# Optimization experiments

Measured on AMD Instinct MI355X. Metric: run time of the kernel, lower is better.

Reference implementation:

```python
import jax, jax.numpy as jnp
import numpy as np

B, N = 16, 4096
NUM_POINTS = (1024, 256)
NUM_SAMPLE = (32, 64)
CH = ((3, 64, 64, 128), (128, 128, 128, 256))


def setup_inputs() -> dict:
    key = jax.random.key(0)
    ks = iter(jax.random.split(key, 64))
    inp = {"points": jax.random.normal(next(ks), (B, 3, N), jnp.float32)}
    for li, ch in enumerate(CH, 1):
        cin = ch[0] + 3  # xyz-offset concat adds 3 channels at layer input
        for ci in range(len(ch) - 1):
            cout = ch[ci + 1]
            inp[f"w{li}{ci}"] = jax.random.normal(next(ks), (cout, cin), jnp.float32) * (1.0 / np.sqrt(cin))
            inp[f"g{li}{ci}"] = 1.0 + 0.1 * jax.random.normal(next(ks), (cout,), jnp.float32)
            inp[f"b{li}{ci}"] = 0.1 * jax.random.normal(next(ks), (cout,), jnp.float32)
            cin = cout
    return inp


def _fps(points_b3n, npoint):
    # furthest point sampling, seeded at index 0 (matches CUDA furthest_point_sample)
    pts = points_b3n.transpose(0, 2, 1)  # [B, N, 3]
    Bc, Nc, _ = pts.shape
    idx0 = jnp.zeros((Bc,), jnp.int32)
    d0 = jnp.full((Bc, Nc), jnp.inf, pts.dtype)

    def step(carry, _):
        dist, last = carry
        lp = jnp.take_along_axis(pts, jnp.broadcast_to(last[:, None, None], (Bc, 1, 3)), axis=1)  # [B,1,3]
        dist = jnp.minimum(dist, jnp.sum((pts - lp) ** 2, -1))
        nxt = jnp.argmax(dist, -1).astype(jnp.int32)
        return (dist, nxt), nxt

    _, rest = jax.lax.scan(step, (d0, idx0), None, length=npoint - 1)
    return jnp.concatenate([idx0[None], rest], 0).T  # [B, npoint]


def _knn(k, points_b3n, query_b3m):
    p = points_b3n.transpose(0, 2, 1)  # [B, N, 3]
    q = query_b3m.transpose(0, 2, 1)   # [B, M, 3]
    d = (jnp.sum(q * q, -1)[:, :, None]
         - 2.0 * jnp.einsum('bmc,bnc->bmn', q, p)
         + jnp.sum(p * p, -1)[:, None, :])  # [B, M, N]
    _, idx = jax.lax.top_k(-d, k)
    return idx  # [B, M, k]


def _group(x_bcn, idx_bmk):
    # gather neighbors: [B, C, N], [B, M, K] -> [B, C, M, K]
    return jax.vmap(lambda x, i: x[:, i])(x_bcn, idx_bmk)


def _forward(points, params):
    feats = points  # feats=None branch
    outs = []
    for npoint, nsample, layer_params in zip(NUM_POINTS, NUM_SAMPLE, params):
        Bc = points.shape[0]
        fps_idx = _fps(points, npoint)  # [B, npoint]
        prop = jnp.take_along_axis(points, jnp.broadcast_to(fps_idx[:, None, :], (Bc, 3, npoint)), axis=2)
        gidx = _knn(nsample, points, prop)  # [B, npoint, nsample]
        gp = _group(points, gidx)           # [B, 3, M, K]
        gpn = gp - prop[..., None]
        gf = _group(feats, gidx)            # [B, C, M, K]
        x = jnp.concatenate([gpn, gf], axis=1)
        for (W, g, b) in layer_params:      # 1x1 Conv2d + folded BN(eval) + ReLU
            x = jnp.einsum('bcmk,oc->bomk', x, W)
            x = jax.nn.relu(x * g[None, :, None, None] + b[None, :, None, None])
        feats = jnp.max(x, axis=-1)  # max-pool over nsample
        points = prop
        outs += [prop, feats]
    return tuple(outs)  # (points1, feats1, points2, feats2)


def reference(points, w10, g10, b10, w11, g11, b11, w12, g12, b12,
              w20, g20, b20, w21, g21, b21, w22, g22, b22):
    params = [[(w10, g10, b10), (w11, g11, b11), (w12, g12, b12)],
              [(w20, g20, b20), (w21, g21, b21), (w22, g22, b22)]]
    return _forward(points, params)
```

## Files before the change

kernel.cpp:

```cpp
#include <hip/hip_runtime.h>
#include <math.h>

#define NB   16

#define O_P1 0
#define O_F1 (16*3*1024)
#define O_P2 (O_F1 + 16*128*1024)
#define O_F2 (O_P2 + 16*3*256)

#define WS_GIDX1 0
#define WS_GIDX2 (WS_GIDX1 + 16*1024*32*4)
#define WS_W1T   (WS_GIDX2 + 16*256*64*4)
#define WS_W2T   (WS_W1T  + 6*64*4)
#define WS_W3T   (WS_W2T  + 64*64*4)
#define WS_W1H   (WS_W3T  + 64*128*4)
#define WS_W2H   (WS_W1H  + 128*160*2)
#define WS_W3H   (WS_W2H  + 128*128*2)
#define WS_PTS4  (WS_W3H  + 256*128*2)
#define WS_P14   (WS_PTS4 + 16*4096*16)

#define DEVINL __device__ __forceinline__
typedef unsigned long long u64;
typedef _Float16 f16x8 __attribute__((ext_vector_type(8)));
typedef float f32x4 __attribute__((ext_vector_type(4)));

DEVINL float4 f4fma(float w, float4 v, float4 a) {
    a.x = fmaf(w, v.x, a.x); a.y = fmaf(w, v.y, a.y);
    a.z = fmaf(w, v.z, a.z); a.w = fmaf(w, v.w, a.w);
    return a;
}
DEVINL float4 f4relub(float4 a, float b) {
    float4 r;
    r.x = fmaxf(a.x + b, 0.f); r.y = fmaxf(a.y + b, 0.f);
    r.z = fmaxf(a.z + b, 0.f); r.w = fmaxf(a.w + b, 0.f);
    return r;
}
DEVINL float f4max(float4 a) { return fmaxf(fmaxf(a.x, a.y), fmaxf(a.z, a.w)); }

DEVINL unsigned fkey(float f) {
    unsigned u = __float_as_uint(f);
    return (u & 0x80000000u) ? ~u : (u | 0x80000000u);
}

DEVINL u64 shflx64(u64 v, int m) {
    unsigned lo = __shfl_xor((unsigned)v, m);
    unsigned hi = __shfl_xor((unsigned)(v >> 32), m);
    return ((u64)hi << 32) | lo;
}

template<int CTRL, int RMASK>
DEVINL unsigned dpp_addstep(unsigned v) {
    unsigned t = (unsigned)__builtin_amdgcn_update_dpp(0, (int)v, CTRL, RMASK, 0xF, true);
    return v + t;
}
DEVINL unsigned wave_scan_add(unsigned v) {
    v = dpp_addstep<0x111, 0xF>(v);
    v = dpp_addstep<0x112, 0xF>(v);
    v = dpp_addstep<0x114, 0xF>(v);
    v = dpp_addstep<0x118, 0xF>(v);
    v = dpp_addstep<0x142, 0xA>(v);
    v = dpp_addstep<0x143, 0xC>(v);
    return v;
}

template<int N, int NP> struct __align__(16) FpsS {
    float4 spts[N];
    int sel[NP];
    u64 rbuf[2][4];
};
struct __align__(16) KnnS {
    unsigned hist[2048];
    unsigned ckey[1024];
    int      cidx[1024];
    unsigned wpart[4];
    unsigned sbin, sKb, scnt, cntL;
};
struct __align__(16) Mlp1S {
    float sw1[6*64], sw2[64*64];
    float sb1[64], sb2[64], sb3[128];
    float sx[6*32], sh1[64*36], sh2[64*36];
    float spm[128*4], sout[128*8];
    int   sgi[32];
    float sq[3];
};

DEVINL void prep_impl(int e0,
    const float* __restrict__ w10, const float* __restrict__ g10,
    const float* __restrict__ w11, const float* __restrict__ g11,
    const float* __restrict__ w12, const float* __restrict__ g12,
    const float* __restrict__ w20, const float* __restrict__ g20,
    const float* __restrict__ w21, const float* __restrict__ g21,
    const float* __restrict__ w22, const float* __restrict__ g22,
    float* __restrict__ w1t, float* __restrict__ w2t, float* __restrict__ w3t,
    _Float16* __restrict__ W1h, _Float16* __restrict__ W2h, _Float16* __restrict__ W3h)
{
    if (e0 < 384)  { int o = e0/6,   i = e0%6;   w1t [i*64  + o] = w10[e0]*g10[o]; return; }
    e0 -= 384;
    if (e0 < 4096) { int o = e0/64,  i = e0%64;  w2t [i*64  + o] = w11[e0]*g11[o]; return; }
    e0 -= 4096;
    if (e0 < 8192) { int o = e0/64,  i = e0%64;  w3t [i*128 + o] = w12[e0]*g12[o]; return; }
    e0 -= 8192;
    if (e0 < 20480){ int o = e0/160, i = e0%160;
                     float v = (i < 131) ? w20[o*131 + i]*g20[o] : 0.f;
                     W1h[e0] = (_Float16)v; return; }
    e0 -= 20480;
    if (e0 < 16384){ W2h[e0] = (_Float16)(w21[e0]*g21[e0/128]); return; }
    e0 -= 16384;
    if (e0 < 32768){ W3h[e0] = (_Float16)(w22[e0]*g22[e0/128]); return; }
}

template<int N, int NP>
DEVINL void fps_impl(FpsS<N, NP>& sm, const float* __restrict__ pts,
                     float* __restrict__ prop, int b, float4* pack_out)
{
    constexpr int NT = 256;
    constexpr int PT = N / NT;
    int tid = threadIdx.x;
    const float* p = pts + (size_t)b * 3 * N;
    for (int n = tid; n < N; n += NT) {
        float x = p[n], y = p[N+n], z = p[2*N+n];
        sm.spts[n] = make_float4(x, y, z, 0.f);
        if (pack_out) {
            float s = __fadd_rn(__fadd_rn(__fmul_rn(x,x), __fmul_rn(y,y)), __fmul_rn(z,z));
            pack_out[(size_t)b*N + n] = make_float4(x, y, z, s);
        }
    }
    __syncthreads();

    float lx[PT], ly[PT], lz[PT], ld[PT];
    int base = tid * PT;
#pragma unroll
    for (int j = 0; j < PT; ++j) {
        float4 q = sm.spts[base+j];
        lx[j] = q.x; ly[j] = q.y; lz[j] = q.z;
        ld[j] = __builtin_inff();
    }
    if (tid == 0) sm.sel[0] = 0;
    float4 qp = sm.spts[0];
    for (int s = 1; s < NP; ++s) {
        float qx = qp.x, qy = qp.y, qz = qp.z;
        float bd = -1.0f; int bi = 0x7FFFFFFF;
#pragma unroll
        for (int j = 0; j < PT; ++j) {
            float dx = __fsub_rn(lx[j], qx);
            float dy = __fsub_rn(ly[j], qy);
            float dz = __fsub_rn(lz[j], qz);
            float dd = __fadd_rn(__fadd_rn(__fmul_rn(dx,dx), __fmul_rn(dy,dy)), __fmul_rn(dz,dz));
            float v = fminf(ld[j], dd);
            ld[j] = v;
            if (v > bd) { bd = v; bi = base + j; }
        }
        u64 pk = ((u64)__float_as_uint(bd) << 32) | (unsigned)(~bi);
#pragma unroll
        for (int mk = 1; mk < 64; mk <<= 1) {
            u64 o = shflx64(pk, mk);
            if (o > pk) pk = o;
        }
        if ((tid & 63) == 0) sm.rbuf[s & 1][tid >> 6] = pk;
        __syncthreads();
        u64 g = sm.rbuf[s & 1][0];
#pragma unroll
        for (int w = 1; w < 4; ++w) { u64 o = sm.rbuf[s & 1][w]; if (o > g) g = o; }
        int last = (int)(~(unsigned)g);
        qp = sm.spts[last];
        if (tid == 0) sm.sel[s] = last;
    }
    __syncthreads();
    for (int m = tid; m < NP; m += NT) {
        float4 q = sm.spts[sm.sel[m]];
        prop[(size_t)b*3*NP + m]        = q.x;
        prop[(size_t)b*3*NP + NP + m]   = q.y;
        prop[(size_t)b*3*NP + 2*NP + m] = q.z;
    }
}

template<int N, int K, int M>
DEVINL void knn_impl(KnnS& sm, const float4* __restrict__ pts4,
                     const float* __restrict__ qry, int* __restrict__ gidx, int bm)
{
    int tid = threadIdx.x, lane = tid & 63, wid = tid >> 6;
    int b = bm / M, m = bm % M;
    const float4* p4 = pts4 + (size_t)b * N;
    float qx = qry[(size_t)b*3*M + m];
    float qy = qry[(size_t)b*3*M + M + m];
    float qz = qry[(size_t)b*3*M + 2*M + m];
    float sqq = __fadd_rn(__fadd_rn(__fmul_rn(qx,qx), __fmul_rn(qy,qy)), __fmul_rn(qz,qz));

    for (int e = tid; e < 2048; e += 256) sm.hist[e] = 0;
    if (tid == 0) { sm.scnt = 0; sm.cntL = 0; sm.sbin = 2047u; sm.sKb = 0; }
    __syncthreads();
    for (int n = tid; n < N; n += 256) {
        float4 pp = p4[n];
        float dot = __fadd_rn(__fadd_rn(__fmul_rn(qx,pp.x), __fmul_rn(qy,pp.y)), __fmul_rn(qz,pp.z));
        float d = __fadd_rn(__fsub_rn(sqq, __fmul_rn(2.0f, dot)), pp.w);
        atomicAdd(&sm.hist[fkey(d) >> 21], 1u);
    }
    __syncthreads();
    unsigned hloc[8], s8 = 0;
#pragma unroll
    for (int j = 0; j < 8; ++j) { hloc[j] = sm.hist[tid*8 + j]; s8 += hloc[j]; }
    unsigned sc = wave_scan_add(s8);
    if (lane == 63) sm.wpart[wid] = sc;
    __syncthreads();
    unsigned woff = 0;
    for (int w = 0; w < wid; ++w) woff += sm.wpart[w];
    unsigned cumEnd = sc + woff;
    unsigned cbase = cumEnd - s8;
    if ((unsigned)K > cbase && (unsigned)K <= cumEnd) {
        unsigned run = cbase;
#pragma unroll
        for (int j = 0; j < 8; ++j) {
            if ((unsigned)K > run && (unsigned)K <= run + hloc[j]) { sm.sbin = (unsigned)(tid*8 + j); sm.sKb = run; }
            run += hloc[j];
        }
    }
    __syncthreads();
    unsigned bin1 = sm.sbin;
    unsigned Kb   = sm.sKb;
    int* gout = gidx + ((size_t)b * M + m) * K;
    for (int n = tid; n < N; n += 256) {
        float4 pp = p4[n];
        float dot = __fadd_rn(__fadd_rn(__fmul_rn(qx,pp.x), __fmul_rn(qy,pp.y)), __fmul_rn(qz,pp.z));
        float d = __fadd_rn(__fsub_rn(sqq, __fmul_rn(2.0f, dot)), pp.w);
        unsigned k = fkey(d), pfx = k >> 21;
        if (pfx < bin1) {
            unsigned pos = atomicAdd(&sm.cntL, 1u);
            if (pos < (unsigned)K) gout[pos] = n;
        } else if (pfx == bin1) {
            unsigned pos = atomicAdd(&sm.scnt, 1u);
            if (pos < 1024u) { sm.ckey[pos] = k; sm.cidx[pos] = n; }
        }
    }
    __syncthreads();
    int cnt = (int)sm.scnt; if (cnt > 1024) cnt = 1024;
    int need = K - (int)Kb;
    if (tid < 64) {
        for (int c = lane; c < cnt; c += 64) {
            unsigned mk = sm.ckey[c]; int mi = sm.cidx[c];
            int rank = 0;
            for (int l = 0; l < cnt; ++l) {
                unsigned ok = sm.ckey[l];
                rank += (ok < mk || (ok == mk && sm.cidx[l] < mi)) ? 1 : 0;
            }
            if (rank < need && (int)Kb + rank < K) gout[Kb + rank] = mi;
        }
    }
}

DEVINL void mlp1_impl(Mlp1S& sm,
    const float* __restrict__ pts,
    const float* __restrict__ q,
    const int*   __restrict__ gidx,
    const float* __restrict__ w1t, const float* __restrict__ w2t, const float* __restrict__ w3t,
    const float* __restrict__ b1, const float* __restrict__ b2, const float* __restrict__ b3,
    float* __restrict__ out, int blk)
{
    int tid = threadIdx.x;
    for (int e = tid; e < 6*64;   e += 256) sm.sw1[e] = w1t[e];
    for (int e = tid; e < 64*64;  e += 256) sm.sw2[e] = w2t[e];
    if (tid < 64) { sm.sb1[tid] = b1[tid]; sm.sb2[tid] = b2[tid]; }
    else if (tid < 192) sm.sb3[tid-64] = b3[tid-64];

    int pid0 = blk * 8;
    int b = pid0 >> 10, m0 = pid0 & 1023;
    int c = tid & 63, kq = tid >> 6, kb = kq * 8;
    __syncthreads();

    for (int it = 0; it < 8; ++it) {
        int m = m0 + it;
        if (tid < 32) sm.sgi[tid] = gidx[((size_t)b*1024 + m)*32 + tid];
        else if (tid < 35) sm.sq[tid-32] = q[((size_t)b*3 + (tid-32))*1024 + m];
        __syncthreads();
        if (tid < 192) {
            int cc = tid >> 5, k = tid & 31;
            int gi = sm.sgi[k];
            const float* pb = pts + (size_t)b*3*4096;
            float v = (cc < 3) ? (pb[cc*4096 + gi] - sm.sq[cc]) : pb[(cc-3)*4096 + gi];
            sm.sx[cc*32 + k] = v;
        }
        __syncthreads();
        float4 a0 = make_float4(0,0,0,0), a1 = make_float4(0,0,0,0);
#pragma unroll
        for (int i = 0; i < 6; ++i) {
            float w = sm.sw1[i*64 + c];
            a0 = f4fma(w, *(const float4*)&sm.sx[i*32 + kb],     a0);
            a1 = f4fma(w, *(const float4*)&sm.sx[i*32 + kb + 4], a1);
        }
        {
            float bias = sm.sb1[c];
            *(float4*)&sm.sh1[c*36 + kb]     = f4relub(a0, bias);
            *(float4*)&sm.sh1[c*36 + kb + 4] = f4relub(a1, bias);
        }
        __syncthreads();
        a0 = make_float4(0,0,0,0); a1 = make_float4(0,0,0,0);
#pragma unroll 4
        for (int i = 0; i < 64; ++i) {
            float w = sm.sw2[i*64 + c];
            a0 = f4fma(w, *(const float4*)&sm.sh1[i*36 + kb],     a0);
            a1 = f4fma(w, *(const float4*)&sm.sh1[i*36 + kb + 4], a1);
        }
        {
            float bias = sm.sb2[c];
            *(float4*)&sm.sh2[c*36 + kb]     = f4relub(a0, bias);
            *(float4*)&sm.sh2[c*36 + kb + 4] = f4relub(a1, bias);
        }
        __syncthreads();
        float4 aA0 = make_float4(0,0,0,0), aA1 = make_float4(0,0,0,0);
        float4 aB0 = make_float4(0,0,0,0), aB1 = make_float4(0,0,0,0);
#pragma unroll 4
        for (int i = 0; i < 64; ++i) {
            float wA = w3t[i*128 + c], wB = w3t[i*128 + c + 64];
            float4 v0 = *(const float4*)&sm.sh2[i*36 + kb];
            float4 v1 = *(const float4*)&sm.sh2[i*36 + kb + 4];
            aA0 = f4fma(wA, v0, aA0); aA1 = f4fma(wA, v1, aA1);
            aB0 = f4fma(wB, v0, aB0); aB1 = f4fma(wB, v1, aB1);
        }
        float mA = fmaxf(fmaxf(f4max(aA0), f4max(aA1)) + sm.sb3[c],      0.f);
        float mB = fmaxf(fmaxf(f4max(aB0), f4max(aB1)) + sm.sb3[c + 64], 0.f);
        sm.spm[c*4 + kq]        = mA;
        sm.spm[(c + 64)*4 + kq] = mB;
        __syncthreads();
        if (tid < 128) {
            float f = fmaxf(fmaxf(sm.spm[tid*4], sm.spm[tid*4+1]), fmaxf(sm.spm[tid*4+2], sm.spm[tid*4+3]));
            sm.sout[tid*8 + it] = f;
        }
        __syncthreads();
    }
    for (int e = tid; e < 128*8; e += 256) {
        int cc = e >> 3, j = e & 7;
        out[((size_t)b*128 + cc)*1024 + m0 + j] = sm.sout[e];
    }
}

__global__ __launch_bounds__(256) void fused1(
    const float* __restrict__ pts, float* __restrict__ p1, float4* __restrict__ pts4,
    const float* w10, const float* g10, const float* w11, const float* g11,
    const float* w12, const float* g12, const float* w20, const float* g20,
    const float* w21, const float* g21, const float* w22, const float* g22,
    float* w1t, float* w2t, float* w3t,
    _Float16* W1h, _Float16* W2h, _Float16* W3h)
{
    __shared__ FpsS<4096, 1024> sm;
    if (blockIdx.x < 16) {
        fps_impl<4096, 1024>(sm, pts, p1, blockIdx.x, nullptr);
    } else if (blockIdx.x < 338) {
        prep_impl((blockIdx.x - 16) * 256 + threadIdx.x,
                  w10, g10, w11, g11, w12, g12, w20, g20, w21, g21, w22, g22,
                  w1t, w2t, w3t, W1h, W2h, W3h);
    } else {
        int pblk = blockIdx.x - 338;
#pragma unroll
        for (int i = 0; i < 4; ++i) {
            int idx = pblk * 1024 + i * 256 + threadIdx.x;
            int b = idx >> 12, n = idx & 4095;
            const float* p = pts + (size_t)b * 3 * 4096;
            float x = p[n], y = p[4096 + n], z = p[2*4096 + n];
            float s = __fadd_rn(__fadd_rn(__fmul_rn(x,x), __fmul_rn(y,y)), __fmul_rn(z,z));
            pts4[idx] = make_float4(x, y, z, s);
        }
    }
}

union SmemK2 { FpsS<1024, 256> fps; KnnS knn; };
__global__ __launch_bounds__(256) void fused2(
    const float4* __restrict__ pts4, const float* __restrict__ p1,
    float* __restrict__ p2, int* __restrict__ gidx1, float4* __restrict__ p14)
{
    __shared__ SmemK2 sm;
    if (blockIdx.x < 16) {
        fps_impl<1024, 256>(sm.fps, p1, p2, blockIdx.x, p14);
    } else {
        knn_impl<4096, 32, 1024>(sm.knn, pts4, p1, gidx1, blockIdx.x - 16);
    }
}

union SmemK3 { Mlp1S mlp; KnnS knn; };
__global__ __launch_bounds__(256) void fused3(
    const float* __restrict__ pts, const float* __restrict__ p1,
    const int* __restrict__ gidx1,
    const float* __restrict__ w1t, const float* __restrict__ w2t, const float* __restrict__ w3t,
    const float* __restrict__ b1, const float* __restrict__ b2, const float* __restrict__ b3,
    float* __restrict__ f1,
    const float4* __restrict__ p14, const float* __restrict__ p2, int* __restrict__ gidx2)
{
    __shared__ SmemK3 sm;
    if (blockIdx.x < 2048) {
        mlp1_impl(sm.mlp, pts, p1, gidx1, w1t, w2t, w3t, b1, b2, b3, f1, blockIdx.x);
    } else {
        knn_impl<1024, 64, 256>(sm.knn, p14, p2, gidx2, blockIdx.x - 2048);
    }
}

__global__ __launch_bounds__(256) void mlp2_kernel(
    const float* __restrict__ p1,
    const float* __restrict__ f1,
    const float* __restrict__ q2,
    const int*   __restrict__ gidx,
    const _Float16* __restrict__ W1h,
    const _Float16* __restrict__ W2h,
    const _Float16* __restrict__ W3h,
    const float* __restrict__ b20, const float* __restrict__ b21, const float* __restrict__ b22,
    float* __restrict__ out)
{
    __shared__ _Float16 xT[64*168];
    __shared__ _Float16 h1T[64*136];
    __shared__ int   sgi[64];
    __shared__ float sq[3];

    int tid = threadIdx.x;
    int b = blockIdx.x >> 8, m = blockIdx.x & 255;
    if (tid < 64) sgi[tid] = gidx[((size_t)b*256 + m)*64 + tid];
    else if (tid < 67) sq[tid-64] = q2[((size_t)b*3 + (tid-64))*256 + m];
    __syncthreads();

    union Pk4 { _Float16 h[4]; u64 u; };
    for (int e = tid; e < 40*64; e += 256) {
        int qi = e >> 6, n = e & 63;
        int gi = sgi[n];
        Pk4 pk;
#pragma unroll
        for (int j = 0; j < 4; ++j) {
            int i = qi*4 + j;
            float v;
            if (i < 3)        v = p1[((size_t)b*3 + i)*1024 + gi] - sq[i];
            else if (i < 131) v = f1[((size_t)b*128 + (i-3))*1024 + gi];
            else              v = 0.f;
            pk.h[j] = (_Float16)v;
        }
        *(u64*)&xT[n*168 + qi*4] = pk.u;
    }
    __syncthreads();

    int wv = tid >> 6, l = tid & 63;
    int lr = l & 15, lk = l >> 4;

    f32x4 acc[2][4];
#pragma unroll
    for (int mi = 0; mi < 2; ++mi)
#pragma unroll
        for (int nt = 0; nt < 4; ++nt) acc[mi][nt] = (f32x4){0.f,0.f,0.f,0.f};
#pragma unroll
    for (int ks = 0; ks < 5; ++ks) {
        int kk = ks*32 + lk*8;
        f16x8 bf[4];
#pragma unroll
        for (int nt = 0; nt < 4; ++nt)
            bf[nt] = *(const f16x8*)&xT[(nt*16 + lr)*168 + kk];
#pragma unroll
        for (int mi = 0; mi < 2; ++mi) {
            f16x8 af = *(const f16x8*)&W1h[(size_t)((wv*2 + mi)*16 + lr)*160 + kk];
#pragma unroll
            for (int nt = 0; nt < 4; ++nt)
                acc[mi][nt] = __builtin_amdgcn_mfma_f32_16x16x32_f16(af, bf[nt], acc[mi][nt], 0, 0, 0);
        }
    }
#pragma unroll
    for (int mi = 0; mi < 2; ++mi) {
        int ch0 = (wv*2 + mi)*16 + lk*4;
        float bb0 = b20[ch0], bb1 = b20[ch0+1], bb2 = b20[ch0+2], bb3 = b20[ch0+3];
#pragma unroll
        for (int nt = 0; nt < 4; ++nt) {
            int n = nt*16 + lr;
            Pk4 pk;
            pk.h[0] = (_Float16)fmaxf(acc[mi][nt][0] + bb0, 0.f);
            pk.h[1] = (_Float16)fmaxf(acc[mi][nt][1] + bb1, 0.f);
            pk.h[2] = (_Float16)fmaxf(acc[mi][nt][2] + bb2, 0.f);
            pk.h[3] = (_Float16)fmaxf(acc[mi][nt][3] + bb3, 0.f);
            *(u64*)&h1T[n*136 + ch0] = pk.u;
        }
    }
    __syncthreads();

    _Float16* h2T = xT;
#pragma unroll
    for (int mi = 0; mi < 2; ++mi)
#pragma unroll
        for (int nt = 0; nt < 4; ++nt) acc[mi][nt] = (f32x4){0.f,0.f,0.f,0.f};
#pragma unroll
    for (int ks = 0; ks < 4; ++ks) {
        int kk = ks*32 + lk*8;
        f16x8 bf[4];
#pragma unroll
        for (int nt = 0; nt < 4; ++nt)
            bf[nt] = *(const f16x8*)&h1T[(nt*16 + lr)*136 + kk];
#pragma unroll
        for (int mi = 0; mi < 2; ++mi) {
            f16x8 af = *(const f16x8*)&W2h[(size_t)((wv*2 + mi)*16 + lr)*128 + kk];
#pragma unroll
            for (int nt = 0; nt < 4; ++nt)
                acc[mi][nt] = __builtin_amdgcn_mfma_f32_16x16x32_f16(af, bf[nt], acc[mi][nt], 0, 0, 0);
        }
    }
    __syncthreads();
#pragma unroll
    for (int mi = 0; mi < 2; ++mi) {
        int ch0 = (wv*2 + mi)*16 + lk*4;
        float bb0 = b21[ch0], bb1 = b21[ch0+1], bb2 = b21[ch0+2], bb3 = b21[ch0+3];
#pragma unroll
        for (int nt = 0; nt < 4; ++nt) {
            int n = nt*16 + lr;
            Pk4 pk;
            pk.h[0] = (_Float16)fmaxf(acc[mi][nt][0] + bb0, 0.f);
            pk.h[1] = (_Float16)fmaxf(acc[mi][nt][1] + bb1, 0.f);
            pk.h[2] = (_Float16)fmaxf(acc[mi][nt][2] + bb2, 0.f);
            pk.h[3] = (_Float16)fmaxf(acc[mi][nt][3] + bb3, 0.f);
            *(u64*)&h2T[n*136 + ch0] = pk.u;
        }
    }
    __syncthreads();

    f32x4 acc3[4][4];
#pragma unroll
    for (int mi = 0; mi < 4; ++mi)
#pragma unroll
        for (int nt = 0; nt < 4; ++nt) acc3[mi][nt] = (f32x4){0.f,0.f,0.f,0.f};
#pragma unroll
    for (int ks = 0; ks < 4; ++ks) {
        int kk = ks*32 + lk*8;
        f16x8 bf[4];
#pragma unroll
        for (int nt = 0; nt < 4; ++nt)
            bf[nt] = *(const f16x8*)&h2T[(nt*16 + lr)*136 + kk];
#pragma unroll
        for (int mi = 0; mi < 4; ++mi) {
            f16x8 af = *(const f16x8*)&W3h[(size_t)((wv*4 + mi)*16 + lr)*128 + kk];
#pragma unroll
            for (int nt = 0; nt < 4; ++nt)
                acc3[mi][nt] = __builtin_amdgcn_mfma_f32_16x16x32_f16(af, bf[nt], acc3[mi][nt], 0, 0, 0);
        }
    }
#pragma unroll
    for (int mi = 0; mi < 4; ++mi) {
        float v0 = acc3[mi][0][0], v1 = acc3[mi][0][1], v2 = acc3[mi][0][2], v3 = acc3[mi][0][3];
#pragma unroll
        for (int nt = 1; nt < 4; ++nt) {
            v0 = fmaxf(v0, acc3[mi][nt][0]);
            v1 = fmaxf(v1, acc3[mi][nt][1]);
            v2 = fmaxf(v2, acc3[mi][nt][2]);
            v3 = fmaxf(v3, acc3[mi][nt][3]);
        }
#pragma unroll
        for (int mk = 1; mk < 16; mk <<= 1) {
            v0 = fmaxf(v0, __shfl_xor(v0, mk));
            v1 = fmaxf(v1, __shfl_xor(v1, mk));
            v2 = fmaxf(v2, __shfl_xor(v2, mk));
            v3 = fmaxf(v3, __shfl_xor(v3, mk));
        }
        if (lr == 0) {
            int ch0 = (wv*4 + mi)*16 + lk*4;
            out[((size_t)b*256 + ch0    )*256 + m] = fmaxf(v0 + b22[ch0],     0.f);
            out[((size_t)b*256 + ch0 + 1)*256 + m] = fmaxf(v1 + b22[ch0 + 1], 0.f);
            out[((size_t)b*256 + ch0 + 2)*256 + m] = fmaxf(v2 + b22[ch0 + 2], 0.f);
            out[((size_t)b*256 + ch0 + 3)*256 + m] = fmaxf(v3 + b22[ch0 + 3], 0.f);
        }
    }
}

extern "C" void kernel_launch(void* const* d_in, const int* in_sizes, int n_in,
                              void* d_out, int out_size, void* d_ws, size_t ws_size,
                              hipStream_t stream)
{
    const float* pts = (const float*)d_in[0];
    const float* w10 = (const float*)d_in[1];
    const float* g10 = (const float*)d_in[2];
    const float* b10 = (const float*)d_in[3];
    const float* w11 = (const float*)d_in[4];
    const float* g11 = (const float*)d_in[5];
    const float* b11 = (const float*)d_in[6];
    const float* w12 = (const float*)d_in[7];
    const float* g12 = (const float*)d_in[8];
    const float* b12 = (const float*)d_in[9];
    const float* w20 = (const float*)d_in[10];
    const float* g20 = (const float*)d_in[11];
    const float* b20 = (const float*)d_in[12];
    const float* w21 = (const float*)d_in[13];
    const float* g21 = (const float*)d_in[14];
    const float* b21 = (const float*)d_in[15];
    const float* w22 = (const float*)d_in[16];
    const float* g22 = (const float*)d_in[17];
    const float* b22 = (const float*)d_in[18];

    float* out = (float*)d_out;
    char* ws = (char*)d_ws;
    int* gidx1 = (int*)(ws + WS_GIDX1);
    int* gidx2 = (int*)(ws + WS_GIDX2);
    float* w1t  = (float*)(ws + WS_W1T);
    float* w2t  = (float*)(ws + WS_W2T);
    float* w3t  = (float*)(ws + WS_W3T);
    _Float16* W1h = (_Float16*)(ws + WS_W1H);
    _Float16* W2h = (_Float16*)(ws + WS_W2H);
    _Float16* W3h = (_Float16*)(ws + WS_W3H);
    float4* pts4 = (float4*)(ws + WS_PTS4);
    float4* p14  = (float4*)(ws + WS_P14);

    float* p1 = out + O_P1;
    float* f1 = out + O_F1;
    float* p2 = out + O_P2;
    float* f2 = out + O_F2;

    fused1<<<16 + 322 + 64, 256, 0, stream>>>(pts, p1, pts4,
                                              w10, g10, w11, g11, w12, g12,
                                              w20, g20, w21, g21, w22, g22,
                                              w1t, w2t, w3t, W1h, W2h, W3h);
    fused2<<<16 + NB * 1024, 256, 0, stream>>>(pts4, p1, p2, gidx1, p14);
    fused3<<<2048 + NB * 256, 256, 0, stream>>>(pts, p1, gidx1,
                                                w1t, w2t, w3t, b10, b11, b12, f1,
                                                p14, p2, gidx2);
    mlp2_kernel<<<NB * 256, 256, 0, stream>>>(p1, f1, p2, gidx2,
                                              W1h, W2h, W3h, b20, b21, b22, f2);
}
```

Baseline: 1.256 ms.

## Rewrite layer-1 MLP with fp16 MFMA and split second kNN into own kernel

Replaces the scalar fp32 FMA layer-1 MLP, which handled one query point per iteration, with an MFMA kernel using fp16 weights prepared in the prep stage. Each block now processes 8 query points (256 neighbors) at once in swizzled LDS tiles, and the max-pool is done with lane shuffles. The second-layer kNN, which previously shared a fused launch with the MLP, is moved to its own kernel launched afterwards. This cuts FP32 ALU work and per-point barriers, but lowers layer-1 precision to fp16 and serializes the kNN after the MLP instead of overlapping them in one launch.

```diff
diff --git a/kernel.cpp b/kernel.cpp
--- a/kernel.cpp
+++ b/kernel.cpp
@@ -10,32 +10,19 @@
 
 #define WS_GIDX1 0
 #define WS_GIDX2 (WS_GIDX1 + 16*1024*32*4)
-#define WS_W1T   (WS_GIDX2 + 16*256*64*4)
-#define WS_W2T   (WS_W1T  + 6*64*4)
-#define WS_W3T   (WS_W2T  + 64*64*4)
-#define WS_W1H   (WS_W3T  + 64*128*4)
+#define WS_W1H   (WS_GIDX2 + 16*256*64*4)
 #define WS_W2H   (WS_W1H  + 128*160*2)
 #define WS_W3H   (WS_W2H  + 128*128*2)
-#define WS_PTS4  (WS_W3H  + 256*128*2)
+#define WS_W1MH  (WS_W3H  + 256*128*2)
+#define WS_W2MH  (WS_W1MH + 64*32*2)
+#define WS_W3MH  (WS_W2MH + 64*64*2)
+#define WS_PTS4  (WS_W3MH + 128*64*2)
 #define WS_P14   (WS_PTS4 + 16*4096*16)
 
 #define DEVINL __device__ __forceinline__
 typedef unsigned long long u64;
 typedef _Float16 f16x8 __attribute__((ext_vector_type(8)));
 typedef float f32x4 __attribute__((ext_vector_type(4)));
-
-DEVINL float4 f4fma(float w, float4 v, float4 a) {
-    a.x = fmaf(w, v.x, a.x); a.y = fmaf(w, v.y, a.y);
-    a.z = fmaf(w, v.z, a.z); a.w = fmaf(w, v.w, a.w);
-    return a;
-}
-DEVINL float4 f4relub(float4 a, float b) {
-    float4 r;
-    r.x = fmaxf(a.x + b, 0.f); r.y = fmaxf(a.y + b, 0.f);
-    r.z = fmaxf(a.z + b, 0.f); r.w = fmaxf(a.w + b, 0.f);
-    return r;
-}
-DEVINL float f4max(float4 a) { return fmaxf(fmaxf(a.x, a.y), fmaxf(a.z, a.w)); }
 
 DEVINL unsigned fkey(float f) {
     unsigned u = __float_as_uint(f);
@@ -61,6 +48,13 @@
     v = dpp_addstep<0x142, 0xA>(v);
     v = dpp_addstep<0x143, 0xC>(v);
     return v;
+}
+
+DEVINL int swz32(int n, int h) {
+    return n*32 + (((h >> 3) ^ (n & 3)) << 3) + (h & 7);
+}
+DEVINL int swz64(int n, int h) {
+    return n*64 + (((h >> 3) ^ (n & 7)) << 3) + (h & 7);
 }
 
 template<int N, int NP> struct __align__(16) FpsS {
@@ -75,14 +69,6 @@
     unsigned wpart[4];
     unsigned sbin, sKb, scnt, cntL;
 };
-struct __align__(16) Mlp1S {
-    float sw1[6*64], sw2[64*64];
-    float sb1[64], sb2[64], sb3[128];
-    float sx[6*32], sh1[64*36], sh2[64*36];
-    float spm[128*4], sout[128*8];
-    int   sgi[32];
-    float sq[3];
-};
 
 DEVINL void prep_impl(int e0,
     const float* __restrict__ w10, const float* __restrict__ g10,
@@ -91,15 +77,9 @@
     const float* __restrict__ w20, const float* __restrict__ g20,
     const float* __restrict__ w21, const float* __restrict__ g21,
     const float* __restrict__ w22, const float* __restrict__ g22,
-    float* __restrict__ w1t, float* __restrict__ w2t, float* __restrict__ w3t,
-    _Float16* __restrict__ W1h, _Float16* __restrict__ W2h, _Float16* __restrict__ W3h)
-{
-    if (e0 < 384)  { int o = e0/6,   i = e0%6;   w1t [i*64  + o] = w10[e0]*g10[o]; return; }
-    e0 -= 384;
-    if (e0 < 4096) { int o = e0/64,  i = e0%64;  w2t [i*64  + o] = w11[e0]*g11[o]; return; }
-    e0 -= 4096;
-    if (e0 < 8192) { int o = e0/64,  i = e0%64;  w3t [i*128 + o] = w12[e0]*g12[o]; return; }
-    e0 -= 8192;
+    _Float16* __restrict__ W1h, _Float16* __restrict__ W2h, _Float16* __restrict__ W3h,
+    _Float16* __restrict__ W1mh, _Float16* __restrict__ W2mh, _Float16* __restrict__ W3mh)
+{
     if (e0 < 20480){ int o = e0/160, i = e0%160;
                      float v = (i < 131) ? w20[o*131 + i]*g20[o] : 0.f;
                      W1h[e0] = (_Float16)v; return; }
@@ -107,6 +87,14 @@
     if (e0 < 16384){ W2h[e0] = (_Float16)(w21[e0]*g21[e0/128]); return; }
     e0 -= 16384;
     if (e0 < 32768){ W3h[e0] = (_Float16)(w22[e0]*g22[e0/128]); return; }
+    e0 -= 32768;
+    if (e0 < 2048) { int o = e0>>5, i = e0&31;
+                     float v = (i < 6) ? w10[o*6 + i]*g10[o] : 0.f;
+                     W1mh[e0] = (_Float16)v; return; }
+    e0 -= 2048;
+    if (e0 < 4096) { W2mh[e0] = (_Float16)(w11[e0]*g11[e0>>6]); return; }
+    e0 -= 4096;
+    if (e0 < 8192) { W3mh[e0] = (_Float16)(w12[e0]*g12[e0>>6]); return; }
 }
 
 template<int N, int NP>
@@ -247,108 +235,23 @@
     }
 }
 
-DEVINL void mlp1_impl(Mlp1S& sm,
-    const float* __restrict__ pts,
-    const float* __restrict__ q,
-    const int*   __restrict__ gidx,
-    const float* __restrict__ w1t, const float* __restrict__ w2t, const float* __restrict__ w3t,
-    const float* __restrict__ b1, const float* __restrict__ b2, const float* __restrict__ b3,
-    float* __restrict__ out, int blk)
-{
-    int tid = threadIdx.x;
-    for (int e = tid; e < 6*64;   e += 256) sm.sw1[e] = w1t[e];
-    for (int e = tid; e < 64*64;  e += 256) sm.sw2[e] = w2t[e];
-    if (tid < 64) { sm.sb1[tid] = b1[tid]; sm.sb2[tid] = b2[tid]; }
-    else if (tid < 192) sm.sb3[tid-64] = b3[tid-64];
-
-    int pid0 = blk * 8;
-    int b = pid0 >> 10, m0 = pid0 & 1023;
-    int c = tid & 63, kq = tid >> 6, kb = kq * 8;
-    __syncthreads();
-
-    for (int it = 0; it < 8; ++it) {
-        int m = m0 + it;
-        if (tid < 32) sm.sgi[tid] = gidx[((size_t)b*1024 + m)*32 + tid];
-        else if (tid < 35) sm.sq[tid-32] = q[((size_t)b*3 + (tid-32))*1024 + m];
-        __syncthreads();
-        if (tid < 192) {
-            int cc = tid >> 5, k = tid & 31;
-            int gi = sm.sgi[k];
-            const float* pb = pts + (size_t)b*3*4096;
-            float v = (cc < 3) ? (pb[cc*4096 + gi] - sm.sq[cc]) : pb[(cc-3)*4096 + gi];
-            sm.sx[cc*32 + k] = v;
-        }
-        __syncthreads();
-        float4 a0 = make_float4(0,0,0,0), a1 = make_float4(0,0,0,0);
-#pragma unroll
-        for (int i = 0; i < 6; ++i) {
-            float w = sm.sw1[i*64 + c];
-            a0 = f4fma(w, *(const float4*)&sm.sx[i*32 + kb],     a0);
-            a1 = f4fma(w, *(const float4*)&sm.sx[i*32 + kb + 4], a1);
-        }
-        {
-            float bias = sm.sb1[c];
-            *(float4*)&sm.sh1[c*36 + kb]     = f4relub(a0, bias);
-            *(float4*)&sm.sh1[c*36 + kb + 4] = f4relub(a1, bias);
-        }
-        __syncthreads();
-        a0 = make_float4(0,0,0,0); a1 = make_float4(0,0,0,0);
-#pragma unroll 4
-        for (int i = 0; i < 64; ++i) {
-            float w = sm.sw2[i*64 + c];
-            a0 = f4fma(w, *(const float4*)&sm.sh1[i*36 + kb],     a0);
-            a1 = f4fma(w, *(const float4*)&sm.sh1[i*36 + kb + 4], a1);
-        }
-        {
-            float bias = sm.sb2[c];
-            *(float4*)&sm.sh2[c*36 + kb]     = f4relub(a0, bias);
-            *(float4*)&sm.sh2[c*36 + kb + 4] = f4relub(a1, bias);
-        }
-        __syncthreads();
-        float4 aA0 = make_float4(0,0,0,0), aA1 = make_float4(0,0,0,0);
-        float4 aB0 = make_float4(0,0,0,0), aB1 = make_float4(0,0,0,0);
-#pragma unroll 4
-        for (int i = 0; i < 64; ++i) {
-            float wA = w3t[i*128 + c], wB = w3t[i*128 + c + 64];
-            float4 v0 = *(const float4*)&sm.sh2[i*36 + kb];
-            float4 v1 = *(const float4*)&sm.sh2[i*36 + kb + 4];
-            aA0 = f4fma(wA, v0, aA0); aA1 = f4fma(wA, v1, aA1);
-            aB0 = f4fma(wB, v0, aB0); aB1 = f4fma(wB, v1, aB1);
-        }
-        float mA = fmaxf(fmaxf(f4max(aA0), f4max(aA1)) + sm.sb3[c],      0.f);
-        float mB = fmaxf(fmaxf(f4max(aB0), f4max(aB1)) + sm.sb3[c + 64], 0.f);
-        sm.spm[c*4 + kq]        = mA;
-        sm.spm[(c + 64)*4 + kq] = mB;
-        __syncthreads();
-        if (tid < 128) {
-            float f = fmaxf(fmaxf(sm.spm[tid*4], sm.spm[tid*4+1]), fmaxf(sm.spm[tid*4+2], sm.spm[tid*4+3]));
-            sm.sout[tid*8 + it] = f;
-        }
-        __syncthreads();
-    }
-    for (int e = tid; e < 128*8; e += 256) {
-        int cc = e >> 3, j = e & 7;
-        out[((size_t)b*128 + cc)*1024 + m0 + j] = sm.sout[e];
-    }
-}
-
 __global__ __launch_bounds__(256) void fused1(
     const float* __restrict__ pts, float* __restrict__ p1, float4* __restrict__ pts4,
     const float* w10, const float* g10, const float* w11, const float* g11,
     const float* w12, const float* g12, const float* w20, const float* g20,
     const float* w21, const float* g21, const float* w22, const float* g22,
-    float* w1t, float* w2t, float* w3t,
-    _Float16* W1h, _Float16* W2h, _Float16* W3h)
+    _Float16* W1h, _Float16* W2h, _Float16* W3h,
+    _Float16* W1mh, _Float16* W2mh, _Float16* W3mh)
 {
     __shared__ FpsS<4096, 1024> sm;
     if (blockIdx.x < 16) {
         fps_impl<4096, 1024>(sm, pts, p1, blockIdx.x, nullptr);
-    } else if (blockIdx.x < 338) {
+    } else if (blockIdx.x < 344) {
         prep_impl((blockIdx.x - 16) * 256 + threadIdx.x,
                   w10, g10, w11, g11, w12, g12, w20, g20, w21, g21, w22, g22,
-                  w1t, w2t, w3t, W1h, W2h, W3h);
+                  W1h, W2h, W3h, W1mh, W2mh, W3mh);
     } else {
-        int pblk = blockIdx.x - 338;
+        int pblk = blockIdx.x - 344;
 #pragma unroll
         for (int i = 0; i < 4; ++i) {
             int idx = pblk * 1024 + i * 256 + threadIdx.x;
@@ -374,21 +277,183 @@
     }
 }
 
-union SmemK3 { Mlp1S mlp; KnnS knn; };
-__global__ __launch_bounds__(256) void fused3(
-    const float* __restrict__ pts, const float* __restrict__ p1,
-    const int* __restrict__ gidx1,
-    const float* __restrict__ w1t, const float* __restrict__ w2t, const float* __restrict__ w3t,
+__global__ __launch_bounds__(256) void mlp1_mfma(
+    const float4* __restrict__ pts4,
+    const float* __restrict__ q,
+    const int*   __restrict__ gidx,
+    const _Float16* __restrict__ W1mh,
+    const _Float16* __restrict__ W2mh,
+    const _Float16* __restrict__ W3mh,
     const float* __restrict__ b1, const float* __restrict__ b2, const float* __restrict__ b3,
-    float* __restrict__ f1,
+    float* __restrict__ out)
+{
+    __shared__ _Float16 xT [256*32];
+    __shared__ _Float16 h1T[256*64];
+    __shared__ float sout[128*8];
+    __shared__ int   sgi[256];
+    __shared__ float sq[24];
+
+    int tid = threadIdx.x;
+    int pid0 = blockIdx.x * 8;
+    int b = pid0 >> 10, m0 = pid0 & 1023;
+
+    sgi[tid] = gidx[((size_t)b*1024 + m0)*32 + tid];
+    if (tid < 24) {
+        int c = tid >> 3, j = tid & 7;
+        sq[tid] = q[((size_t)b*3 + c)*1024 + m0 + j];
+    }
+    __syncthreads();
+
+    union Pk4 { _Float16 h[4]; u64 u; };
+    {
+        int n = tid, pos = n >> 5;
+        float4 pp = pts4[(size_t)b*4096 + sgi[n]];
+        float v[8];
+        v[0] = pp.x - sq[pos]; v[1] = pp.y - sq[8+pos]; v[2] = pp.z - sq[16+pos];
+        v[3] = pp.x; v[4] = pp.y; v[5] = pp.z; v[6] = 0.f; v[7] = 0.f;
+#pragma unroll
+        for (int qi = 0; qi < 8; ++qi) {
+            Pk4 pk;
+            if (qi < 2) {
+#pragma unroll
+                for (int j = 0; j < 4; ++j) pk.h[j] = (_Float16)v[qi*4 + j];
+            } else pk.u = 0;
+            *(u64*)&xT[swz32(n, qi*4)] = pk.u;
+        }
+    }
+    __syncthreads();
+
+    int wv = tid >> 6, l = tid & 63;
+    int lr = l & 15, lk = l >> 4;
+
+    f32x4 acc[4][4];
+#pragma unroll
+    for (int mi = 0; mi < 4; ++mi)
+#pragma unroll
+        for (int nt = 0; nt < 4; ++nt) acc[mi][nt] = (f32x4){0.f,0.f,0.f,0.f};
+    {
+        int kk = lk*8;
+        f16x8 bf[4];
+#pragma unroll
+        for (int nt = 0; nt < 4; ++nt)
+            bf[nt] = *(const f16x8*)&xT[swz32((4*wv + nt)*16 + lr, kk)];
+#pragma unroll
+        for (int mi = 0; mi < 4; ++mi) {
+            f16x8 af = *(const f16x8*)&W1mh[(mi*16 + lr)*32 + kk];
+#pragma unroll
+            for (int nt = 0; nt < 4; ++nt)
+                acc[mi][nt] = __builtin_amdgcn_mfma_f32_16x16x32_f16(af, bf[nt], acc[mi][nt], 0, 0, 0);
+        }
+    }
+#pragma unroll
+    for (int mi = 0; mi < 4; ++mi) {
+        int ch0 = mi*16 + lk*4;
+        float bb0 = b1[ch0], bb1 = b1[ch0+1], bb2 = b1[ch0+2], bb3 = b1[ch0+3];
+#pragma unroll
+        for (int nt = 0; nt < 4; ++nt) {
+            int n = (4*wv + nt)*16 + lr;
+            Pk4 pk;
+            pk.h[0] = (_Float16)fmaxf(acc[mi][nt][0] + bb0, 0.f);
+            pk.h[1] = (_Float16)fmaxf(acc[mi][nt][1] + bb1, 0.f);
+            pk.h[2] = (_Float16)fmaxf(acc[mi][nt][2] + bb2, 0.f);
+            pk.h[3] = (_Float16)fmaxf(acc[mi][nt][3] + bb3, 0.f);
+            *(u64*)&h1T[swz64(n, ch0)] = pk.u;
+        }
+    }
+
+#pragma unroll
+    for (int mi = 0; mi < 4; ++mi)
+#pragma unroll
+        for (int nt = 0; nt < 4; ++nt) acc[mi][nt] = (f32x4){0.f,0.f,0.f,0.f};
+#pragma unroll
+    for (int ks = 0; ks < 2; ++ks) {
+        int kk = ks*32 + lk*8;
+        f16x8 bf[4];
+#pragma unroll
+        for (int nt = 0; nt < 4; ++nt)
+            bf[nt] = *(const f16x8*)&h1T[swz64((4*wv + nt)*16 + lr, kk)];
+#pragma unroll
+        for (int mi = 0; mi < 4; ++mi) {
+            f16x8 af = *(const f16x8*)&W2mh[(mi*16 + lr)*64 + kk];
+#pragma unroll
+            for (int nt = 0; nt < 4; ++nt)
+                acc[mi][nt] = __builtin_amdgcn_mfma_f32_16x16x32_f16(af, bf[nt], acc[mi][nt], 0, 0, 0);
+        }
+    }
+#pragma unroll
+    for (int mi = 0; mi < 4; ++mi) {
+        int ch0 = mi*16 + lk*4;
+        float bb0 = b2[ch0], bb1 = b2[ch0+1], bb2 = b2[ch0+2], bb3 = b2[ch0+3];
+#pragma unroll
+        for (int nt = 0; nt < 4; ++nt) {
+            int n = (4*wv + nt)*16 + lr;
+            Pk4 pk;
+            pk.h[0] = (_Float16)fmaxf(acc[mi][nt][0] + bb0, 0.f);
+            pk.h[1] = (_Float16)fmaxf(acc[mi][nt][1] + bb1, 0.f);
+            pk.h[2] = (_Float16)fmaxf(acc[mi][nt][2] + bb2, 0.f);
+            pk.h[3] = (_Float16)fmaxf(acc[mi][nt][3] + bb3, 0.f);
+            *(u64*)&h1T[swz64(n, ch0)] = pk.u;
+        }
+    }
+
+    f32x4 acc3[8][4];
+#pragma unroll
+    for (int mi = 0; mi < 8; ++mi)
+#pragma unroll
+        for (int nt = 0; nt < 4; ++nt) acc3[mi][nt] = (f32x4){0.f,0.f,0.f,0.f};
+#pragma unroll
+    for (int ks = 0; ks < 2; ++ks) {
+        int kk = ks*32 + lk*8;
+        f16x8 bf[4];
+#pragma unroll
+        for (int nt = 0; nt < 4; ++nt)
+            bf[nt] = *(const f16x8*)&h1T[swz64((4*wv + nt)*16 + lr, kk)];
+#pragma unroll
+        for (int mi = 0; mi < 8; ++mi) {
+            f16x8 af = *(const f16x8*)&W3mh[(mi*16 + lr)*64 + kk];
+#pragma unroll
+            for (int nt = 0; nt < 4; ++nt)
+                acc3[mi][nt] = __builtin_amdgcn_mfma_f32_16x16x32_f16(af, bf[nt], acc3[mi][nt], 0, 0, 0);
+        }
+    }
+#pragma unroll
+    for (int mi = 0; mi < 8; ++mi) {
+        float va[4], vb[4];
+#pragma unroll
+        for (int r = 0; r < 4; ++r) {
+            va[r] = fmaxf(acc3[mi][0][r], acc3[mi][1][r]);
+            vb[r] = fmaxf(acc3[mi][2][r], acc3[mi][3][r]);
+        }
+#pragma unroll
+        for (int mk = 1; mk < 16; mk <<= 1) {
+#pragma unroll
+            for (int r = 0; r < 4; ++r) {
+                va[r] = fmaxf(va[r], __shfl_xor(va[r], mk));
+                vb[r] = fmaxf(vb[r], __shfl_xor(vb[r], mk));
+            }
+        }
+        if (lr == 0) {
+            int ch0 = mi*16 + lk*4;
+#pragma unroll
+            for (int r = 0; r < 4; ++r) {
+                float bias = b3[ch0 + r];
+                sout[(ch0 + r)*8 + 2*wv    ] = fmaxf(va[r] + bias, 0.f);
+                sout[(ch0 + r)*8 + 2*wv + 1] = fmaxf(vb[r] + bias, 0.f);
+            }
+        }
+    }
+    __syncthreads();
+    for (int e = tid; e < 128*8; e += 256) {
+        int cc = e >> 3, j = e & 7;
+        out[((size_t)b*128 + cc)*1024 + m0 + j] = sout[e];
+    }
+}
+
+__global__ __launch_bounds__(256) void knn2_kernel(
     const float4* __restrict__ p14, const float* __restrict__ p2, int* __restrict__ gidx2)
 {
-    __shared__ SmemK3 sm;
-    if (blockIdx.x < 2048) {
-        mlp1_impl(sm.mlp, pts, p1, gidx1, w1t, w2t, w3t, b1, b2, b3, f1, blockIdx.x);
-    } else {
-        knn_impl<1024, 64, 256>(sm.knn, p14, p2, gidx2, blockIdx.x - 2048);
-    }
+    __shared__ KnnS sm;
+    knn_impl<1024, 64, 256>(sm, p14, p2, gidx2, blockIdx.x);
 }
 
 __global__ __launch_bounds__(256) void mlp2_kernel(
@@ -584,12 +649,12 @@
     char* ws = (char*)d_ws;
     int* gidx1 = (int*)(ws + WS_GIDX1);
     int* gidx2 = (int*)(ws + WS_GIDX2);
-    float* w1t  = (float*)(ws + WS_W1T);
-    float* w2t  = (float*)(ws + WS_W2T);
-    float* w3t  = (float*)(ws + WS_W3T);
-    _Float16* W1h = (_Float16*)(ws + WS_W1H);
-    _Float16* W2h = (_Float16*)(ws + WS_W2H);
-    _Float16* W3h = (_Float16*)(ws + WS_W3H);
+    _Float16* W1h  = (_Float16*)(ws + WS_W1H);
+    _Float16* W2h  = (_Float16*)(ws + WS_W2H);
+    _Float16* W3h  = (_Float16*)(ws + WS_W3H);
+    _Float16* W1mh = (_Float16*)(ws + WS_W1MH);
+    _Float16* W2mh = (_Float16*)(ws + WS_W2MH);
+    _Float16* W3mh = (_Float16*)(ws + WS_W3MH);
     float4* pts4 = (float4*)(ws + WS_PTS4);
     float4* p14  = (float4*)(ws + WS_P14);
 
@@ -598,14 +663,14 @@
     float* p2 = out + O_P2;
     float* f2 = out + O_F2;
 
-    fused1<<<16 + 322 + 64, 256, 0, stream>>>(pts, p1, pts4,
+    fused1<<<16 + 328 + 64, 256, 0, stream>>>(pts, p1, pts4,
                                               w10, g10, w11, g11, w12, g12,
                                               w20, g20, w21, g21, w22, g22,
-                                              w1t, w2t, w3t, W1h, W2h, W3h);
+                                              W1h, W2h, W3h, W1mh, W2mh, W3mh);
     fused2<<<16 + NB * 1024, 256, 0, stream>>>(pts4, p1, p2, gidx1, p14);
-    fused3<<<2048 + NB * 256, 256, 0, stream>>>(pts, p1, gidx1,
-                                                w1t, w2t, w3t, b10, b11, b12, f1,
-                                                p14, p2, gidx2);
+    mlp1_mfma<<<NB * 128, 256, 0, stream>>>(pts4, p1, gidx1,
+                                            W1mh, W2mh, W3mh, b10, b11, b12, f1);
+    knn2_kernel<<<NB * 256, 256, 0, stream>>>(p14, p2, gidx2);
     mlp2_kernel<<<NB * 256, 256, 0, stream>>>(p1, f1, p2, gidx2,
                                               W1h, W2h, W3h, b20, b21, b22, f2);
 }
```

New measurement: 1.123 ms (median of 2 runs). -10.5%, faster.
